# Performance work log

Measured on AMD Instinct MI355X. Metric: run time of the kernel, lower is better.

## Reference

```python
import jax, jax.numpy as jnp
import numpy as np
import math

N_HEADS = 4
N_KV_GROUPS = 1
HEAD_DIM = 256
SLIDING_WINDOW = 512
ROPE_BASE = 1000000.0
EPS = 1e-6


def _rmsnorm(x, gamma):
    # normalize over last dim (head_dim), torch nn.RMSNorm semantics
    ms = jnp.mean(jnp.square(x), axis=-1, keepdims=True)
    return x * jax.lax.rsqrt(ms + EPS) * gamma


def _rope_tables(T, head_dim, dtype):
    inv_freq = 1.0 / (ROPE_BASE ** (jnp.arange(0, head_dim, 2, dtype=jnp.float32) / head_dim))
    t = jnp.arange(T, dtype=jnp.float32)
    freqs = jnp.outer(t, inv_freq)          # [T, head_dim/2]
    return jnp.cos(freqs).astype(dtype), jnp.sin(freqs).astype(dtype)


def _apply_rope(x, cos, sin):
    # x: [B, T, H, hd]; cos/sin: [T, hd/2] broadcast as [1, T, 1, hd/2]
    x0 = x[..., 0::2]
    x1 = x[..., 1::2]
    c = cos[None, :, None, :]
    s = sin[None, :, None, :]
    even = x0 * c - x1 * s
    odd = x0 * s + x1 * c
    return jnp.stack((even, odd), axis=-1).reshape(x.shape)


def setup_inputs() -> dict:
    key = jax.random.key(0)
    ks = jax.random.split(key, 5)
    B, T, C = 2, 4096, 1024
    scale = 0.02
    return {
        "x": jax.random.normal(ks[0], (B, T, C), dtype=jnp.float32),
        "Wq": jax.random.normal(ks[1], (C, C), dtype=jnp.float32) * scale,
        "Wk": jax.random.normal(ks[2], (N_KV_GROUPS * HEAD_DIM, C), dtype=jnp.float32) * scale,
        "Wv": jax.random.normal(ks[3], (N_KV_GROUPS * HEAD_DIM, C), dtype=jnp.float32) * scale,
        "Wo": jax.random.normal(ks[4], (C, C), dtype=jnp.float32) * scale,
        "q_gamma": jnp.ones((HEAD_DIM,), dtype=jnp.float32),
        "k_gamma": jnp.ones((HEAD_DIM,), dtype=jnp.float32),
    }


def reference(x, Wq, Wk, Wv, Wo, q_gamma, k_gamma):
    B, T, C = x.shape
    H, G, hd = N_HEADS, N_KV_GROUPS, HEAD_DIM
    rep = H // G

    q = (x @ Wq.T).reshape(B, T, H, hd)
    k = (x @ Wk.T).reshape(B, T, G, hd)
    v = (x @ Wv.T).reshape(B, T, G, hd)

    q = _rmsnorm(q, q_gamma)
    k = _rmsnorm(k, k_gamma)

    cos, sin = _rope_tables(T, hd, q.dtype)
    q = _apply_rope(q, cos, sin)
    k = _apply_rope(k, cos, sin)

    q = q.transpose(0, 2, 1, 3)                 # [B, H, T, hd]
    k = k.transpose(0, 2, 1, 3)                 # [B, G, T, hd]
    v = v.transpose(0, 2, 1, 3)
    k = jnp.repeat(k, rep, axis=1)              # [B, H, T, hd]
    v = jnp.repeat(v, rep, axis=1)

    scores = jnp.einsum("bhqd,bhkd->bhqk", q, k) / math.sqrt(hd)
    i = jnp.arange(T)[:, None]
    j = jnp.arange(T)[None, :]
    allowed = (j <= i) & (j >= i - SLIDING_WINDOW)   # causal sliding window
    scores = jnp.where(allowed, scores, -jnp.inf)
    attn = jax.nn.softmax(scores, axis=-1)
    out = jnp.einsum("bhqk,bhkd->bhqd", attn, v)     # [B, H, T, hd]
    out = out.transpose(0, 2, 1, 3).reshape(B, T, C)
    return out @ Wo.T
```

## Files before the change

kernel.cpp:

```cpp
#include <hip/hip_runtime.h>
#include <cstdint>
#include <cstddef>

#define T_SEQ 4096
#define NB    2
#define CDIM  1024
#define HD    256
#define NH    4

typedef __attribute__((ext_vector_type(8))) __bf16 bf16x8;
typedef __attribute__((ext_vector_type(4))) __bf16 bf16x4;
typedef __attribute__((ext_vector_type(4))) float  floatx4;

__device__ __forceinline__ floatx4 mfma16(bf16x8 a, bf16x8 b, floatx4 c) {
  return __builtin_amdgcn_mfma_f32_16x16x32_bf16(a, b, c, 0, 0, 0);
}

__device__ __forceinline__ void gl2lds16(const void* g, void* l) {
  __builtin_amdgcn_global_load_lds(
      (__attribute__((address_space(1))) void*)g,
      (__attribute__((address_space(3))) void*)l, 16, 0, 0);
}

__global__ __launch_bounds__(256) void cvt_all(const float* __restrict__ x,
                                               const float* __restrict__ wq,
                                               const float* __restrict__ wk,
                                               const float* __restrict__ wv,
                                               const float* __restrict__ wo,
                                               __bf16* __restrict__ xb,
                                               __bf16* __restrict__ wb,
                                               __bf16* __restrict__ wob) {
  int i = blockIdx.x * 256 + threadIdx.x;
  const float* src;
  __bf16* dst;
  int off;
  if (i < 2097152)      { src = x;  dst = xb;            off = i; }
  else if (i < 2359296) { src = wq; dst = wb;            off = i - 2097152; }
  else if (i < 2424832) { src = wk; dst = wb + 1048576;  off = i - 2359296; }
  else if (i < 2490368) { src = wv; dst = wb + 1310720;  off = i - 2424832; }
  else                  { src = wo; dst = wob;           off = i - 2490368; }
  float4 v = ((const float4*)src)[off];
  bf16x4 o;
  o[0] = (__bf16)v.x; o[1] = (__bf16)v.y; o[2] = (__bf16)v.z; o[3] = (__bf16)v.w;
  *(bf16x4*)&dst[(size_t)off * 4] = o;
}

template <typename OutT>
__global__ __launch_bounds__(256) void gemm_bt(const __bf16* __restrict__ A,
                                               const __bf16* __restrict__ B,
                                               OutT* __restrict__ C,
                                               int M, int N, int K) {
  __shared__ __bf16 As[128 * 64];
  __shared__ __bf16 Bs[128 * 64];
  const int tid  = threadIdx.x;
  const int lane = tid & 63;
  const int wave = tid >> 6;
  const int wm = wave >> 1, wn = wave & 1;
  const int lrow = lane & 15, quad = lane >> 4;
  const int bm = blockIdx.y, bn = blockIdx.x;

  const __bf16* gA = A + (size_t)(bm * 128) * K;
  const __bf16* gB = B + (size_t)(bn * 128) * K;
  const int arow = tid >> 3;
  const int acol = ((tid & 7) ^ ((tid >> 3) & 7)) * 8;
  const int l7 = lrow & 7;

  floatx4 acc[4][4] = {};

  for (int kt = 0; kt < K; kt += 64) {
#pragma unroll
    for (int i = 0; i < 4; ++i)
      gl2lds16(gA + (size_t)(i * 32 + arow) * K + kt + acol, &As[i * 2048 + tid * 8]);
#pragma unroll
    for (int i = 0; i < 4; ++i)
      gl2lds16(gB + (size_t)(i * 32 + arow) * K + kt + acol, &Bs[i * 2048 + tid * 8]);
    __syncthreads();
#pragma unroll
    for (int kk = 0; kk < 2; ++kk) {
      bf16x8 af[4], bfr[4];
#pragma unroll
      for (int mi = 0; mi < 4; ++mi)
        af[mi] = *(const bf16x8*)&As[(wm * 64 + mi * 16 + lrow) * 64 +
                                     ((kk * 4 + quad) ^ l7) * 8];
#pragma unroll
      for (int ni = 0; ni < 4; ++ni)
        bfr[ni] = *(const bf16x8*)&Bs[(wn * 64 + ni * 16 + lrow) * 64 +
                                      ((kk * 4 + quad) ^ l7) * 8];
#pragma unroll
      for (int mi = 0; mi < 4; ++mi)
#pragma unroll
        for (int ni = 0; ni < 4; ++ni)
          acc[mi][ni] = mfma16(af[mi], bfr[ni], acc[mi][ni]);
    }
    __syncthreads();
  }

  const int row0 = bm * 128 + wm * 64;
  const int col0 = bn * 128 + wn * 64;
#pragma unroll
  for (int mi = 0; mi < 4; ++mi)
#pragma unroll
    for (int ni = 0; ni < 4; ++ni)
#pragma unroll
      for (int r = 0; r < 4; ++r) {
        int row = row0 + mi * 16 + quad * 4 + r;
        int col = col0 + ni * 16 + lrow;
        C[(size_t)row * N + col] = (OutT)acc[mi][ni][r];
      }
}

__global__ __launch_bounds__(256) void rmsrope(const __bf16* __restrict__ qkv,
                                               const float* __restrict__ qg,
                                               const float* __restrict__ kg,
                                               __bf16* __restrict__ qr,
                                               __bf16* __restrict__ kr,
                                               __bf16* __restrict__ vt) {
  __shared__ __bf16 Ls[64 * 256];
  if (blockIdx.x >= 5120) {
    const int vb = blockIdx.x - 5120;
    const int b = vb >> 6, tt = vb & 63;
    const int tid = threadIdx.x;
    const __bf16* src = qkv + ((size_t)(b * 4096 + tt * 64)) * 1536 + 1280;
#pragma unroll
    for (int i = 0; i < 8; ++i)
      gl2lds16(src + (size_t)(i * 8 + (tid >> 5)) * 1536 + (tid & 31) * 8,
               &Ls[i * 2048 + tid * 8]);
    __syncthreads();
    __bf16 buf[64];
#pragma unroll
    for (int i = 0; i < 64; ++i) buf[i] = Ls[i * 256 + tid];
    __bf16* dst = vt + ((size_t)(b * 256 + tid)) * T_SEQ + tt * 64;
#pragma unroll
    for (int i = 0; i < 8; ++i)
      *(bf16x8*)&dst[i * 8] = *(const bf16x8*)&buf[i * 8];
    return;
  }

  const int inst = blockIdx.x * 4 + (threadIdx.x >> 6);
  const int lane = threadIdx.x & 63;
  const int rp = inst / 5, which = inst - rp * 5;
  const int row = rp * 2 + (lane >> 5);
  const int hl = lane & 31;
  const int b = row >> 12, t = row & 4095;

  const int srcoff = (which < 4) ? which * 256 : 1024;
  const __bf16* src = qkv + (size_t)row * 1536 + srcoff;
  bf16x8 xv = *(const bf16x8*)&src[hl * 8];

  float xf[8];
  float ss = 0.f;
#pragma unroll
  for (int j = 0; j < 8; ++j) { xf[j] = (float)xv[j]; ss += xf[j] * xf[j]; }
#pragma unroll
  for (int off = 16; off >= 1; off >>= 1) ss += __shfl_xor(ss, off);
  const float rms = rsqrtf(ss * (1.0f / 256.0f) + 1e-6f);

  const float* g = (which < 4) ? qg : kg;
  const float4 gv0 = *(const float4*)&g[hl * 8];
  const float4 gv1 = *(const float4*)&g[hl * 8 + 4];
  float y[8];
  y[0] = xf[0] * rms * gv0.x; y[1] = xf[1] * rms * gv0.y;
  y[2] = xf[2] * rms * gv0.z; y[3] = xf[3] * rms * gv0.w;
  y[4] = xf[4] * rms * gv1.x; y[5] = xf[5] * rms * gv1.y;
  y[6] = xf[6] * rms * gv1.z; y[7] = xf[7] * rms * gv1.w;

  const float c_log2 = -19.931568569324174f / 128.0f;
  bf16x8 ov;
#pragma unroll
  for (int j = 0; j < 4; ++j) {
    const int p = hl * 4 + j;
    const float a = (float)t * exp2f((float)p * c_log2);
    const float sn = __sinf(a), cs = __cosf(a);
    ov[2 * j]     = (__bf16)(y[2 * j] * cs - y[2 * j + 1] * sn);
    ov[2 * j + 1] = (__bf16)(y[2 * j] * sn + y[2 * j + 1] * cs);
  }

  __bf16* dst = (which < 4)
      ? qr + ((size_t)((b * NH + which) * T_SEQ) + t) * 256
      : kr + ((size_t)(b * T_SEQ) + t) * 256;
  *(bf16x8*)&dst[hl * 8] = ov;
}

__global__ __launch_bounds__(512, 4) void attn(const __bf16* __restrict__ qr,
                                               const __bf16* __restrict__ kr,
                                               const __bf16* __restrict__ vt,
                                               __bf16* __restrict__ ao) {
  __shared__ __bf16 Ks[2][32 * 256];
  __shared__ __bf16 Vs[2][256 * 32];
  __shared__ __bf16 Ps[2][64 * 32];

  const int bid = ((blockIdx.x & 7) << 6) | (blockIdx.x >> 3);
  const int qi = bid & 63, h = (bid >> 6) & 3, b = bid >> 8;
  const int tid = threadIdx.x, wave = tid >> 6, lane = tid & 63;
  const int lrow = lane & 15, quad = lane >> 4;
  const int l7 = lrow & 7;

  const __bf16* Q = qr + (size_t)((b * NH + h) * T_SEQ) * 256;
  const __bf16* K = kr + (size_t)(b * T_SEQ) * 256;
  const __bf16* V = vt + (size_t)(b * 256) * T_SEQ;

  const int qbase = qi * 64;
  const int jt0 = (qi >= 8) ? 2 * qi - 16 : 0;
  const int jt1 = 2 * qi + 1;
  const int NT = jt1 - jt0 + 1;

  if (wave < 4) {
    const int kb = wave & 1, qh = wave >> 1;
    const int t = tid;
    const int krow = t >> 5;
    const int kcol = ((t & 31) ^ krow) * 8;

    bf16x8 qf[2][8];
#pragma unroll
    for (int qt = 0; qt < 2; ++qt)
#pragma unroll
      for (int c = 0; c < 8; ++c)
        qf[qt][c] = *(const bf16x8*)&Q[(size_t)(qbase + qh * 32 + qt * 16 + lrow) * 256 +
                                       c * 32 + quad * 8];

#pragma unroll
    for (int i = 0; i < 4; ++i)
      gl2lds16(K + (size_t)(jt0 * 32 + i * 8 + krow) * 256 + kcol,
               &Ks[jt0 & 1][i * 2048 + t * 8]);

    for (int jt = jt0; jt <= jt1; ++jt) {
      if (jt < jt1) {
#pragma unroll
        for (int i = 0; i < 4; ++i)
          gl2lds16(K + (size_t)((jt + 1) * 32 + i * 8 + krow) * 256 + kcol,
                   &Ks[(jt + 1) & 1][i * 2048 + t * 8]);
        asm volatile("s_waitcnt vmcnt(4)" ::: "memory");
      } else {
        asm volatile("s_waitcnt vmcnt(0)" ::: "memory");
      }

      const __bf16* Kb = Ks[jt & 1];
      floatx4 s[2] = {};
      __builtin_amdgcn_s_setprio(1);
#pragma unroll
      for (int c = 0; c < 8; ++c) {
        bf16x8 kf = *(const bf16x8*)&Kb[(kb * 16 + lrow) * 256 +
                                        ((c * 4 + quad) ^ l7) * 8];
        s[0] = mfma16(kf, qf[0][c], s[0]);
        s[1] = mfma16(kf, qf[1][c], s[1]);
      }
      __builtin_amdgcn_s_setprio(0);

      const bool full = (jt <= 2 * qi - 1) && (jt >= 2 * qi - 14);
      const float C1 = 0.09016844005556021f;
      const float C2 = 23.083120654223415f;
      __bf16* Pb = Ps[jt & 1];
#pragma unroll
      for (int qt = 0; qt < 2; ++qt) {
        bf16x4 pk;
#pragma unroll
        for (int r = 0; r < 4; ++r) {
          float v = s[qt][r];
          if (!full) {
            const int jk = jt * 32 + kb * 16 + quad * 4 + r;
            const int iq = qbase + qh * 32 + qt * 16 + lrow;
            v = ((jk <= iq) && (jk + 512 >= iq)) ? v : -1e30f;
          }
          pk[r] = (__bf16)exp2f(v * C1 - C2);
        }
        const int q = qh * 32 + qt * 16 + lrow;
        const int chunk = (kb * 2 + (quad >> 1)) ^ ((q ^ (q >> 2)) & 3);
        *(bf16x4*)((char*)Pb + q * 64 + chunk * 16 + (quad & 1) * 8) = pk;
      }
      asm volatile("s_waitcnt lgkmcnt(0)\n\ts_barrier" ::: "memory");
    }
  } else {
    const int dw = wave - 4;
    const int t = tid - 256;
    const int vrow4 = t >> 2;
    const int vcol = ((t & 3) ^ ((vrow4 ^ (vrow4 >> 2)) & 3)) * 8;

    bf16x8 onesv;
#pragma unroll
    for (int j = 0; j < 8; ++j) onesv[j] = (__bf16)1.0f;

    floatx4 o[4][4] = {};
    floatx4 lm[4] = {};

    for (int ii = 0; ii <= NT; ++ii) {
      const int jt = jt0 + ii;
      const int jp = jt - 1;
      if (jt <= jt1) {
#pragma unroll
        for (int i = 0; i < 4; ++i)
          gl2lds16(V + (size_t)(i * 64 + vrow4) * T_SEQ + jt * 32 + vcol,
                   &Vs[jt & 1][i * 2048 + t * 8]);
        asm volatile("s_waitcnt vmcnt(4)" ::: "memory");
      } else {
        asm volatile("s_waitcnt vmcnt(0)" ::: "memory");
      }

      if (ii >= 1) {
        const __bf16* Pb = Ps[jp & 1];
        const __bf16* Vb = Vs[jp & 1];
        bf16x8 pf[4];
#pragma unroll
        for (int qt = 0; qt < 4; ++qt) {
          const int q = qt * 16 + lrow;
          pf[qt] = *(const bf16x8*)((char*)Pb + q * 64 +
                                    (quad ^ ((q ^ (q >> 2)) & 3)) * 16);
        }
        __builtin_amdgcn_s_setprio(1);
#pragma unroll
        for (int qt = 0; qt < 4; ++qt) lm[qt] = mfma16(pf[qt], onesv, lm[qt]);
#pragma unroll
        for (int n = 0; n < 4; ++n) {
          const int row = dw * 64 + n * 16 + lrow;
          bf16x8 vf = *(const bf16x8*)&Vb[row * 32 +
                                          ((quad ^ ((row ^ (row >> 2)) & 3)) * 8)];
#pragma unroll
          for (int qt = 0; qt < 4; ++qt)
            o[qt][n] = mfma16(pf[qt], vf, o[qt][n]);
        }
        __builtin_amdgcn_s_setprio(0);
      }
      if (ii < NT)
        asm volatile("s_waitcnt lgkmcnt(0)\n\ts_barrier" ::: "memory");
    }

#pragma unroll
    for (int qt = 0; qt < 4; ++qt)
#pragma unroll
      for (int r = 0; r < 4; ++r) {
        const float rl = 1.0f / lm[qt][r];
        const int tg = qbase + qt * 16 + quad * 4 + r;
#pragma unroll
        for (int n = 0; n < 4; ++n)
          ao[((size_t)(b * T_SEQ + tg)) * CDIM + h * 256 + dw * 64 + n * 16 + lrow] =
              (__bf16)(o[qt][n][r] * rl);
      }
  }
}

extern "C" void kernel_launch(void* const* d_in, const int* in_sizes, int n_in,
                              void* d_out, int out_size, void* d_ws, size_t ws_size,
                              hipStream_t stream) {
  const float* x  = (const float*)d_in[0];
  const float* Wq = (const float*)d_in[1];
  const float* Wk = (const float*)d_in[2];
  const float* Wv = (const float*)d_in[3];
  const float* Wo = (const float*)d_in[4];
  const float* qg = (const float*)d_in[5];
  const float* kg = (const float*)d_in[6];
  float* out = (float*)d_out;

  const size_t M = (size_t)NB * T_SEQ;
  char* ws = (char*)d_ws;
  __bf16* xb  = (__bf16*)ws; ws += M * CDIM * 2;
  __bf16* wb  = (__bf16*)ws; ws += (size_t)1536 * CDIM * 2;
  __bf16* wob = (__bf16*)ws; ws += (size_t)CDIM * CDIM * 2;
  __bf16* qkv = (__bf16*)ws; ws += M * 1536 * 2;
  __bf16* qr  = (__bf16*)ws; ws += M * CDIM * 2;
  __bf16* kr  = (__bf16*)ws; ws += M * HD * 2;
  __bf16* vt  = (__bf16*)ws; ws += M * HD * 2;
  __bf16* ao  = (__bf16*)ws;

  cvt_all<<<10752, 256, 0, stream>>>(x, Wq, Wk, Wv, Wo, xb, wb, wob);

  gemm_bt<__bf16><<<dim3(12, 64), 256, 0, stream>>>(xb, wb, qkv, 8192, 1536, 1024);

  rmsrope<<<5248, 256, 0, stream>>>(qkv, qg, kg, qr, kr, vt);

  attn<<<NB * NH * (T_SEQ / 64), 512, 0, stream>>>(qr, kr, vt, ao);

  gemm_bt<float><<<dim3(8, 64), 256, 0, stream>>>(ao, wob, out, 8192, 1024, 1024);
}
```

Measured before the change: 205.3 us.

## Triple-buffer K and V tiles in attention with a two-ahead prefetch

```diff
diff --git a/kernel.cpp b/kernel.cpp
--- a/kernel.cpp
+++ b/kernel.cpp
@@ -181,12 +181,12 @@
   *(bf16x8*)&dst[hl * 8] = ov;
 }
 
-__global__ __launch_bounds__(512, 4) void attn(const __bf16* __restrict__ qr,
+__global__ __launch_bounds__(512, 2) void attn(const __bf16* __restrict__ qr,
                                                const __bf16* __restrict__ kr,
                                                const __bf16* __restrict__ vt,
                                                __bf16* __restrict__ ao) {
-  __shared__ __bf16 Ks[2][32 * 256];
-  __shared__ __bf16 Vs[2][256 * 32];
+  __shared__ __bf16 Ks[3][32 * 256];
+  __shared__ __bf16 Vs[3][256 * 32];
   __shared__ __bf16 Ps[2][64 * 32];
 
   const int bid = ((blockIdx.x & 7) << 6) | (blockIdx.x >> 3);
@@ -221,20 +221,22 @@
 #pragma unroll
     for (int i = 0; i < 4; ++i)
       gl2lds16(K + (size_t)(jt0 * 32 + i * 8 + krow) * 256 + kcol,
-               &Ks[jt0 & 1][i * 2048 + t * 8]);
+               &Ks[jt0 % 3][i * 2048 + t * 8]);
+#pragma unroll
+    for (int i = 0; i < 4; ++i)
+      gl2lds16(K + (size_t)((jt0 + 1) * 32 + i * 8 + krow) * 256 + kcol,
+               &Ks[(jt0 + 1) % 3][i * 2048 + t * 8]);
+    asm volatile("s_waitcnt vmcnt(4)\n\ts_barrier" ::: "memory");
 
     for (int jt = jt0; jt <= jt1; ++jt) {
-      if (jt < jt1) {
+      if (jt + 2 <= jt1) {
 #pragma unroll
         for (int i = 0; i < 4; ++i)
-          gl2lds16(K + (size_t)((jt + 1) * 32 + i * 8 + krow) * 256 + kcol,
-                   &Ks[(jt + 1) & 1][i * 2048 + t * 8]);
-        asm volatile("s_waitcnt vmcnt(4)" ::: "memory");
-      } else {
-        asm volatile("s_waitcnt vmcnt(0)" ::: "memory");
-      }
-
-      const __bf16* Kb = Ks[jt & 1];
+          gl2lds16(K + (size_t)((jt + 2) * 32 + i * 8 + krow) * 256 + kcol,
+                   &Ks[(jt + 2) % 3][i * 2048 + t * 8]);
+      }
+
+      const __bf16* Kb = Ks[jt % 3];
       floatx4 s[2] = {};
       __builtin_amdgcn_s_setprio(1);
 #pragma unroll
@@ -267,7 +269,10 @@
         const int chunk = (kb * 2 + (quad >> 1)) ^ ((q ^ (q >> 2)) & 3);
         *(bf16x4*)((char*)Pb + q * 64 + chunk * 16 + (quad & 1) * 8) = pk;
       }
-      asm volatile("s_waitcnt lgkmcnt(0)\n\ts_barrier" ::: "memory");
+      if (jt + 2 <= jt1)
+        asm volatile("s_waitcnt lgkmcnt(0) vmcnt(4)\n\ts_barrier" ::: "memory");
+      else
+        asm volatile("s_waitcnt lgkmcnt(0) vmcnt(0)\n\ts_barrier" ::: "memory");
     }
   } else {
     const int dw = wave - 4;
@@ -282,22 +287,26 @@
     floatx4 o[4][4] = {};
     floatx4 lm[4] = {};
 
+#pragma unroll
+    for (int i = 0; i < 4; ++i)
+      gl2lds16(V + (size_t)(i * 64 + vrow4) * T_SEQ + jt0 * 32 + vcol,
+               &Vs[jt0 % 3][i * 2048 + t * 8]);
+    asm volatile("s_barrier" ::: "memory");
+
     for (int ii = 0; ii <= NT; ++ii) {
-      const int jt = jt0 + ii;
-      const int jp = jt - 1;
-      if (jt <= jt1) {
+      const int jv = jt0 + ii + 1;
+      const int jp = jt0 + ii - 1;
+      const bool stg = (jv <= jt1);
+      if (stg) {
 #pragma unroll
         for (int i = 0; i < 4; ++i)
-          gl2lds16(V + (size_t)(i * 64 + vrow4) * T_SEQ + jt * 32 + vcol,
-                   &Vs[jt & 1][i * 2048 + t * 8]);
-        asm volatile("s_waitcnt vmcnt(4)" ::: "memory");
-      } else {
-        asm volatile("s_waitcnt vmcnt(0)" ::: "memory");
+          gl2lds16(V + (size_t)(i * 64 + vrow4) * T_SEQ + jv * 32 + vcol,
+                   &Vs[jv % 3][i * 2048 + t * 8]);
       }
 
       if (ii >= 1) {
         const __bf16* Pb = Ps[jp & 1];
-        const __bf16* Vb = Vs[jp & 1];
+        const __bf16* Vb = Vs[jp % 3];
         bf16x8 pf[4];
 #pragma unroll
         for (int qt = 0; qt < 4; ++qt) {
@@ -319,8 +328,13 @@
         }
         __builtin_amdgcn_s_setprio(0);
       }
-      if (ii < NT)
-        asm volatile("s_waitcnt lgkmcnt(0)\n\ts_barrier" ::: "memory");
+
+      if (ii < NT) {
+        if (stg)
+          asm volatile("s_waitcnt vmcnt(4)\n\ts_barrier" ::: "memory");
+        else
+          asm volatile("s_waitcnt vmcnt(0)\n\ts_barrier" ::: "memory");
+      }
     }
 
 #pragma unroll
```

After: 218.5 us. 6.5% more time.
